# Kernel tuning notes

Measured on AMD Instinct MI355X. Metric: run time of the kernel, lower is better.

The kernel has to match this reference:

```python
import jax, jax.numpy as jnp
import numpy as np

B, S, Q, D = 8, 2048, 2048, 1024  # additive path requires S == Q


def setup_inputs() -> dict:
    key = jax.random.key(0)
    ks = jax.random.split(key, 5)
    def glorot(k, shape):
        fan_in, fan_out = shape[0], shape[1]
        limit = np.sqrt(6.0 / (fan_in + fan_out)).astype(np.float32)
        return jax.random.uniform(k, shape, jnp.float32, -limit, limit)
    return {
        "source": jax.random.normal(ks[0], (B, S, D), jnp.float32),
        "query": jax.random.normal(ks[1], (B, Q, D), jnp.float32),
        "kernel": glorot(ks[2], (S, Q)),
        "wk_kernel": glorot(ks[3], (D, Q)),
        "wq_kernel": glorot(ks[4], (S, D)),
    }


def reference(source, query, kernel, wk_kernel, wq_kernel):
    # query permuted to (B, D, Q) as in call()
    q_t = jnp.transpose(query, (0, 2, 1))
    # additive similarity: tanh(Wk . Source + Wq . Query) . kernel
    f_att = (jnp.einsum("bsd,dq->bsq", source, wk_kernel)
             + jnp.einsum("sd,bdq->bsq", wq_kernel, q_t))  # (B, S, Q)
    sim = jnp.einsum("bsq,qt->bst", jnp.tanh(f_att), kernel)  # (B, S, Q)
    sm = jax.nn.softmax(sim, axis=-1)  # softmax over last axis (Keras default)
    # sm_t = permute(sm, (0,2,1)); result = batch_dot(sm_t, Source)
    return jnp.einsum("bsq,bsd->bqd", sm, source)  # (B, Q, D)
```

## Files before the change

kernel.cpp:

```cpp
#include <hip/hip_runtime.h>
#include <hip/hip_bf16.h>
#include <stdint.h>

typedef unsigned short u16;

#define B_ 8
#define S_ 2048
#define Q_ 2048
#define D_ 1024
#define T_ 2048

typedef __attribute__((ext_vector_type(8))) short short8;
typedef __attribute__((ext_vector_type(16))) float f32x16;

__device__ __forceinline__ u16 f2b(float f) {
  union { float f; uint32_t u; } x; x.f = f;
  uint32_t r = x.u + 0x7fffu + ((x.u >> 16) & 1u);
  return (u16)(r >> 16);
}
__device__ __forceinline__ float b2f(u16 h) {
  union { uint32_t u; float f; } x; x.u = ((uint32_t)h) << 16;
  return x.f;
}
__device__ __forceinline__ float tanh_fast(float x) {
  return 1.0f - 2.0f / (__expf(2.0f * x) + 1.0f);
}
__device__ __forceinline__ void async16(const void* g, void* l) {
  __builtin_amdgcn_global_load_lds(
      (const __attribute__((address_space(1))) void*)g,
      (__attribute__((address_space(3))) void*)l, 16, 0, 0);
}

__global__ void cast_f32_bf16_k(const float* __restrict__ in, u16* __restrict__ out, int n4) {
  int i = blockIdx.x * 256 + threadIdx.x;
  if (i >= n4) return;
  float4 v = ((const float4*)in)[i];
  uint32_t lo = (uint32_t)f2b(v.x) | ((uint32_t)f2b(v.y) << 16);
  uint32_t hi = (uint32_t)f2b(v.z) | ((uint32_t)f2b(v.w) << 16);
  ((uint2*)out)[i] = make_uint2(lo, hi);
}

__global__ void transpose_f32_bf16_v(const float* __restrict__ in, u16* __restrict__ out,
                                     int R, int C) {
  __shared__ u16 t[64 * 72];
  int z = blockIdx.z;
  const float* pin = in + (size_t)z * R * C;
  u16* pout = out + (size_t)z * R * C;
  int c0 = blockIdx.x * 64, r0 = blockIdx.y * 64;
  int tid = threadIdx.x;
  int rr = tid >> 4, c4 = (tid & 15) * 4;
#pragma unroll
  for (int p = 0; p < 4; ++p) {
    int r = p * 16 + rr;
    float4 v = *(const float4*)&pin[(size_t)(r0 + r) * C + c0 + c4];
    t[(c4 + 0) * 72 + r] = f2b(v.x);
    t[(c4 + 1) * 72 + r] = f2b(v.y);
    t[(c4 + 2) * 72 + r] = f2b(v.z);
    t[(c4 + 3) * 72 + r] = f2b(v.w);
  }
  __syncthreads();
  int ct = tid >> 3, r8 = (tid & 7) * 8;
#pragma unroll
  for (int p = 0; p < 2; ++p) {
    int c = p * 32 + ct;
    uint2 lo = *(const uint2*)&t[c * 72 + r8];
    uint2 hi = *(const uint2*)&t[c * 72 + r8 + 4];
    *(uint4*)&pout[(size_t)(c0 + c) * R + r0 + r8] = make_uint4(lo.x, lo.y, hi.x, hi.y);
  }
}

__global__ void src_prep_v(const float* __restrict__ in, u16* __restrict__ outc,
                           u16* __restrict__ outT) {
  __shared__ u16 t[64 * 72];
  int z = blockIdx.z;
  const float* pin = in + (size_t)z * S_ * D_;
  u16* pc = outc + (size_t)z * S_ * D_;
  u16* pt = outT + (size_t)z * S_ * D_;
  int c0 = blockIdx.x * 64, r0 = blockIdx.y * 64;
  int tid = threadIdx.x;
  int rr = tid >> 4, c4 = (tid & 15) * 4;
#pragma unroll
  for (int p = 0; p < 4; ++p) {
    int r = p * 16 + rr;
    float4 v = *(const float4*)&pin[(size_t)(r0 + r) * D_ + c0 + c4];
    u16 b0 = f2b(v.x), b1 = f2b(v.y), b2 = f2b(v.z), b3 = f2b(v.w);
    uint2 pk;
    pk.x = (uint32_t)b0 | ((uint32_t)b1 << 16);
    pk.y = (uint32_t)b2 | ((uint32_t)b3 << 16);
    *(uint2*)&pc[(size_t)(r0 + r) * D_ + c0 + c4] = pk;
    t[(c4 + 0) * 72 + r] = b0;
    t[(c4 + 1) * 72 + r] = b1;
    t[(c4 + 2) * 72 + r] = b2;
    t[(c4 + 3) * 72 + r] = b3;
  }
  __syncthreads();
  int ct = tid >> 3, r8 = (tid & 7) * 8;
#pragma unroll
  for (int p = 0; p < 2; ++p) {
    int c = p * 32 + ct;
    uint2 lo = *(const uint2*)&t[c * 72 + r8];
    uint2 hi = *(const uint2*)&t[c * 72 + r8 + 4];
    *(uint4*)&pt[(size_t)(c0 + c) * S_ + r0 + r8] = make_uint4(lo.x, lo.y, hi.x, hi.y);
  }
}

__global__ void scale_srcT_k(u16* __restrict__ srcT, const float* __restrict__ l) {
  size_t i = (size_t)blockIdx.x * 256 + threadIdx.x;
  size_t e0 = i * 8;
  int s8 = (int)(e0 & (S_ - 1));
  int bb = (int)(e0 / ((size_t)D_ * S_));
  const float* lp = l + (size_t)bb * S_ + s8;
  float4 l0 = *(const float4*)lp;
  float4 l1 = *(const float4*)(lp + 4);
  uint4 raw = *(uint4*)&srcT[e0];
  uint32_t w[4] = {raw.x, raw.y, raw.z, raw.w};
  float li[8] = {l0.x, l0.y, l0.z, l0.w, l1.x, l1.y, l1.z, l1.w};
  uint32_t o[4];
#pragma unroll
  for (int k = 0; k < 4; ++k) {
    float a = b2f((u16)(w[k] & 0xffffu)) / li[2 * k];
    float b = b2f((u16)(w[k] >> 16)) / li[2 * k + 1];
    o[k] = (uint32_t)f2b(a) | ((uint32_t)f2b(b) << 16);
  }
  *(uint4*)&srcT[e0] = make_uint4(o[0], o[1], o[2], o[3]);
}

__global__ __launch_bounds__(512, 2) void gemm256_k(
    const u16* __restrict__ A1, long lda1, long bsA1,
    const u16* __restrict__ B1, long ldb1, long bsB1,
    const u16* __restrict__ A2, long lda2, long bsA2,
    const u16* __restrict__ B2, long ldb2, long bsB2,
    void* __restrict__ Cv, long ldc, long bsC,
    int K, int Srows, int nTerms, int mode, float* __restrict__ lsum) {
  __shared__ __align__(16) u16 lds[65536];

  const int tid = threadIdx.x;
  const int w = tid >> 6, lane = tid & 63;
  const int wr = w >> 2, wc = w & 3;
  const int l31 = lane & 31, hi = lane >> 5;

  const int gx = gridDim.x;
  const int nwg = gx * (int)gridDim.y;
  int lid = blockIdx.y * gx + blockIdx.x;
  if ((nwg & 7) == 0) lid = (lid & 7) * (nwg >> 3) + (lid >> 3);
  const int bn = lid % gx, bm = lid / gx;
  const int n0 = bn * 256, m0 = bm * 256;
  const int b = m0 / Srows;
  const int s0 = m0 - b * Srows;

  const int ktiles = K >> 6;
  const int ktlog = __ffs(ktiles) - 1;
  const int ktmask = ktiles - 1;
  const int NT = nTerms * ktiles;

  const u16* gA1 = A1 + (size_t)bsA1 * b + (size_t)s0 * lda1;
  const u16* gB1 = B1 + (size_t)bsB1 * b + (size_t)n0 * ldb1;
  const u16* gA2 = (nTerms > 1) ? (A2 + (size_t)bsA2 * b + (size_t)s0 * lda2) : gA1;
  const u16* gB2 = (nTerms > 1) ? (B2 + (size_t)bsB2 * b + (size_t)n0 * ldb2) : gB1;

  const int lrow = lane >> 3, lslot = lane & 7;
  const int gsl = (lslot ^ lrow) << 3;

  auto STG = [&](int tile, int isB, int half) {
    if (tile >= NT) return;
    const int term = tile >> ktlog;
    const int kt = (tile & ktmask) << 6;
    const u16* g = isB ? (term ? gB2 : gB1) : (term ? gA2 : gA1);
    const long ld = isB ? (term ? ldb2 : ldb1) : (term ? lda2 : lda1);
    u16* lb = lds + ((tile & 1) << 15) + (isB << 14);
#pragma unroll
    for (int is = 0; is < 2; ++is) {
      const int rh0 = is * 64 + w * 8;
      const int r0 = isB ? (half * 32 + (rh0 & 31) + ((rh0 >> 5) << 6))
                         : (half * 64 + (rh0 & 63) + ((rh0 >> 6) << 7));
      async16(g + (size_t)(r0 + lrow) * ld + kt + gsl, lb + r0 * 64);
    }
  };

  f32x16 acc[4][2];
#pragma unroll
  for (int x = 0; x < 4; ++x)
#pragma unroll
    for (int y = 0; y < 2; ++y)
#pragma unroll
      for (int r = 0; r < 16; ++r) acc[x][y][r] = 0.0f;

  u16* bufXA = lds;
  u16* bufXB = lds + 16384;
  u16* bufYA = lds + 32768;
  u16* bufYB = lds + 49152;

  const int aR = (wr * 128 + l31) * 64;
  const int bR = (wc * 64 + l31) * 64;
  int soff[4];
#pragma unroll
  for (int kk = 0; kk < 4; ++kk)
    soff[kk] = ((((kk << 1) | hi) ^ (l31 & 7)) << 3);

  short8 av[2][4], bv[4];

#define RD_A(bufA, mh)                                                        \
  _Pragma("unroll") for (int m = 0; m < 2; ++m)                               \
  _Pragma("unroll") for (int kk = 0; kk < 4; ++kk)                            \
      av[m][kk] = *(const short8*)&(bufA)[aR + ((mh)*2 + m) * 2048 + soff[kk]];
#define RD_B(bufB, nh)                                                        \
  _Pragma("unroll") for (int kk = 0; kk < 4; ++kk)                            \
      bv[kk] = *(const short8*)&(bufB)[bR + (nh)*2048 + soff[kk]];
#define BAR                              \
  __builtin_amdgcn_sched_barrier(0);     \
  __builtin_amdgcn_s_barrier();          \
  __builtin_amdgcn_sched_barrier(0)
#define MFMA8(mh, nh)                                                         \
  __builtin_amdgcn_s_setprio(1);                                              \
  _Pragma("unroll") for (int kk = 0; kk < 4; ++kk)                            \
  _Pragma("unroll") for (int m = 0; m < 2; ++m)                               \
      acc[(mh)*2 + m][nh] = __builtin_amdgcn_mfma_f32_32x32x16_bf16(          \
          av[m][kk], bv[kk], acc[(mh)*2 + m][nh], 0, 0, 0);                   \
  __builtin_amdgcn_s_setprio(0)
#define VMC4                                         \
  asm volatile("s_waitcnt vmcnt(4)" ::: "memory");   \
  __builtin_amdgcn_sched_barrier(0)

  STG(0, 0, 0); STG(0, 1, 1); STG(0, 0, 1); STG(0, 1, 0);
  STG(1, 0, 0); STG(1, 1, 1);
  VMC4;
  BAR;

  const int niter = NT >> 1;
  for (int i = 0; i < niter; ++i) {
    const int u = 2 * i;
    RD_A(bufXA, 0); RD_B(bufXB, 0);
    STG(u + 1, 0, 1);
    BAR; MFMA8(0, 0); BAR;

    RD_B(bufXB, 1);
    STG(u + 1, 1, 0);
    BAR; MFMA8(0, 1); BAR;

    RD_A(bufXA, 1);
    STG(u + 2, 0, 0);
    BAR; MFMA8(1, 1); BAR;

    RD_B(bufXB, 0);
    STG(u + 2, 1, 1);
    BAR; MFMA8(1, 0);
    VMC4;
    BAR;

    RD_A(bufYA, 0); RD_B(bufYB, 0);
    STG(u + 2, 0, 1);
    BAR; MFMA8(0, 0); BAR;

    RD_B(bufYB, 1);
    STG(u + 2, 1, 0);
    BAR; MFMA8(0, 1); BAR;

    RD_A(bufYA, 1);
    STG(u + 3, 0, 0);
    BAR; MFMA8(1, 1); BAR;

    RD_B(bufYB, 0);
    STG(u + 3, 1, 1);
    BAR; MFMA8(1, 0);
    VMC4;
    BAR;
  }

  if (mode == 3) {
#pragma unroll
    for (int mi = 0; mi < 4; ++mi)
#pragma unroll
      for (int ni = 0; ni < 2; ++ni)
#pragma unroll
        for (int r = 0; r < 16; ++r) acc[mi][ni][r] = __expf(acc[mi][ni][r]);
    float* lrowp = lsum + (size_t)b * Srows + s0;
#pragma unroll
    for (int mi = 0; mi < 4; ++mi)
#pragma unroll
      for (int r = 0; r < 16; ++r) {
        float pv = acc[mi][0][r] + acc[mi][1][r];
        pv += __shfl_xor(pv, 1);
        pv += __shfl_xor(pv, 2);
        pv += __shfl_xor(pv, 4);
        pv += __shfl_xor(pv, 8);
        pv += __shfl_xor(pv, 16);
        if (l31 == 0) {
          const int row = wr * 128 + mi * 32 + (r & 3) + 8 * (r >> 2) + 4 * hi;
          atomicAdd(&lrowp[row], pv);
        }
      }
    u16* gP = (u16*)Cv + (size_t)bsC * b + (size_t)n0 * ldc + s0;
    __syncthreads();
#pragma unroll
    for (int p = 0; p < 2; ++p) {
      if ((wc >> 1) == p) {
#pragma unroll
        for (int mi = 0; mi < 4; ++mi)
#pragma unroll
          for (int ni = 0; ni < 2; ++ni) {
            const int tc = (wc & 1) * 64 + ni * 32 + l31;
#pragma unroll
            for (int g2 = 0; g2 < 4; ++g2) {
              const int sr = wr * 128 + mi * 32 + g2 * 8 + hi * 4;
              u16 p0 = f2b(acc[mi][ni][g2 * 4 + 0]);
              u16 p1 = f2b(acc[mi][ni][g2 * 4 + 1]);
              u16 p2 = f2b(acc[mi][ni][g2 * 4 + 2]);
              u16 p3 = f2b(acc[mi][ni][g2 * 4 + 3]);
              uint2 pk;
              pk.x = (uint32_t)p0 | ((uint32_t)p1 << 16);
              pk.y = (uint32_t)p2 | ((uint32_t)p3 << 16);
              *(uint2*)&lds[tc * 268 + sr] = pk;
            }
          }
      }
      __syncthreads();
#pragma unroll
      for (int j = 0; j < 8; ++j) {
        const int idx = j * 512 + tid;
        const int tt = idx >> 5, s8 = (idx & 31) * 8;
        uint2 lo = *(const uint2*)&lds[tt * 268 + s8];
        uint2 h2 = *(const uint2*)&lds[tt * 268 + s8 + 4];
        *(uint4*)&gP[(size_t)(p * 128 + tt) * ldc + s8] =
            make_uint4(lo.x, lo.y, h2.x, h2.y);
      }
      __syncthreads();
    }
    return;
  }

  const size_t cb = (size_t)bsC * b + (size_t)s0 * ldc + n0;
  if (mode == 2) {
    float* C = (float*)Cv + cb;
#pragma unroll
    for (int mi = 0; mi < 4; ++mi)
#pragma unroll
      for (int ni = 0; ni < 2; ++ni) {
        const int col = wc * 64 + ni * 32 + l31;
#pragma unroll
        for (int r = 0; r < 16; ++r) {
          const int row = wr * 128 + mi * 32 + (r & 3) + 8 * (r >> 2) + 4 * hi;
          C[(size_t)row * ldc + col] = acc[mi][ni][r];
        }
      }
  } else {
    u16* C = (u16*)Cv + cb;
#pragma unroll
    for (int mi = 0; mi < 4; ++mi)
#pragma unroll
      for (int ni = 0; ni < 2; ++ni) {
        const int col = wc * 64 + ni * 32 + l31;
#pragma unroll
        for (int r = 0; r < 16; ++r) {
          const int row = wr * 128 + mi * 32 + (r & 3) + 8 * (r >> 2) + 4 * hi;
          float v = acc[mi][ni][r];
          if (mode == 0) v = tanh_fast(v);
          C[(size_t)row * ldc + col] = f2b(v);
        }
      }
  }
}

#undef RD_A
#undef RD_B
#undef BAR
#undef MFMA8
#undef VMC4

extern "C" void kernel_launch(void* const* d_in, const int* in_sizes, int n_in,
                              void* d_out, int out_size, void* d_ws, size_t ws_size,
                              hipStream_t stream) {
  const float* src = (const float*)d_in[0];
  const float* qry = (const float*)d_in[1];
  const float* ker = (const float*)d_in[2];
  const float* wk  = (const float*)d_in[3];
  const float* wq  = (const float*)d_in[4];
  float* out = (float*)d_out;
  u16* ws = (u16*)d_ws;

  u16* srcb  = ws;
  u16* qryb  = srcb  + (size_t)B_ * S_ * D_;
  u16* wqb   = qryb  + (size_t)B_ * Q_ * D_;
  u16* wkT   = wqb   + (size_t)S_ * D_;
  u16* kerT  = wkT   + (size_t)D_ * Q_;
  u16* srcT  = kerT  + (size_t)Q_ * T_;
  u16* tanhT = srcT  + (size_t)B_ * D_ * S_;
  u16* PT    = tanhT + (size_t)B_ * S_ * Q_;
  float* l   = (float*)(PT + (size_t)B_ * T_ * S_);

  dim3 tb(256);

  cast_f32_bf16_k<<<(B_ * Q_ * D_) / 1024, 256, 0, stream>>>(qry, qryb, (B_ * Q_ * D_) / 4);
  cast_f32_bf16_k<<<(S_ * D_) / 1024, 256, 0, stream>>>(wq, wqb, (S_ * D_) / 4);
  transpose_f32_bf16_v<<<dim3(Q_ / 64, D_ / 64, 1), tb, 0, stream>>>(wk, wkT, D_, Q_);
  transpose_f32_bf16_v<<<dim3(T_ / 64, Q_ / 64, 1), tb, 0, stream>>>(ker, kerT, Q_, T_);
  src_prep_v<<<dim3(D_ / 64, S_ / 64, B_), tb, 0, stream>>>(src, srcb, srcT);
  hipMemsetAsync(l, 0, (size_t)B_ * S_ * sizeof(float), stream);

  gemm256_k<<<dim3(Q_ / 256, (B_ * S_) / 256), 512, 0, stream>>>(
      srcb, D_, (long)S_ * D_,
      wkT, D_, 0,
      wqb, D_, 0,
      qryb, D_, (long)Q_ * D_,
      tanhT, Q_, (long)S_ * Q_,
      D_, S_, 2, 0, nullptr);

  gemm256_k<<<dim3(T_ / 256, (B_ * S_) / 256), 512, 0, stream>>>(
      tanhT, Q_, (long)S_ * Q_,
      kerT, Q_, 0,
      nullptr, 0, 0, nullptr, 0, 0,
      PT, S_, (long)T_ * S_,
      Q_, S_, 1, 3, l);

  scale_srcT_k<<<(B_ * D_ * S_) / (256 * 8), 256, 0, stream>>>(srcT, l);

  gemm256_k<<<dim3(D_ / 256, (B_ * T_) / 256), 512, 0, stream>>>(
      PT, S_, (long)T_ * S_,
      srcT, S_, (long)D_ * S_,
      nullptr, 0, 0, nullptr, 0, 0,
      out, D_, (long)T_ * D_,
      S_, T_, 1, 2, nullptr);
}
```

Before: 629.9 us.

## Pad LDS tile rows, peel the last K iteration, and tighten waitcnt scheduling

```diff
diff --git a/kernel.cpp b/kernel.cpp
--- a/kernel.cpp
+++ b/kernel.cpp
@@ -132,7 +132,7 @@
     const u16* __restrict__ B2, long ldb2, long bsB2,
     void* __restrict__ Cv, long ldc, long bsC,
     int K, int Srows, int nTerms, int mode, float* __restrict__ lsum) {
-  __shared__ __align__(16) u16 lds[65536];
+  __shared__ __align__(16) u16 lds[67584];
 
   const int tid = threadIdx.x;
   const int w = tid >> 6, lane = tid & 63;
@@ -167,13 +167,13 @@
     const int kt = (tile & ktmask) << 6;
     const u16* g = isB ? (term ? gB2 : gB1) : (term ? gA2 : gA1);
     const long ld = isB ? (term ? ldb2 : ldb1) : (term ? lda2 : lda1);
-    u16* lb = lds + ((tile & 1) << 15) + (isB << 14);
+    u16* lb = lds + (tile & 1) * 33792 + isB * 16896;
 #pragma unroll
     for (int is = 0; is < 2; ++is) {
       const int rh0 = is * 64 + w * 8;
       const int r0 = isB ? (half * 32 + (rh0 & 31) + ((rh0 >> 5) << 6))
                          : (half * 64 + (rh0 & 63) + ((rh0 >> 6) << 7));
-      async16(g + (size_t)(r0 + lrow) * ld + kt + gsl, lb + r0 * 64);
+      async16(g + (size_t)(r0 + lrow) * ld + kt + gsl, lb + (r0 >> 3) * 528);
     }
   };
 
@@ -186,12 +186,12 @@
       for (int r = 0; r < 16; ++r) acc[x][y][r] = 0.0f;
 
   u16* bufXA = lds;
-  u16* bufXB = lds + 16384;
-  u16* bufYA = lds + 32768;
-  u16* bufYB = lds + 49152;
-
-  const int aR = (wr * 128 + l31) * 64;
-  const int bR = (wc * 64 + l31) * 64;
+  u16* bufXB = lds + 16896;
+  u16* bufYA = lds + 33792;
+  u16* bufYB = lds + 50688;
+
+  const int aBase = (wr * 16 + (l31 >> 3)) * 528 + (l31 & 7) * 64;
+  const int bBase = (wc * 8 + (l31 >> 3)) * 528 + (l31 & 7) * 64;
   int soff[4];
 #pragma unroll
   for (int kk = 0; kk < 4; ++kk)
@@ -199,17 +199,25 @@
 
   short8 av[2][4], bv[4];
 
-#define RD_A(bufA, mh)                                                        \
-  _Pragma("unroll") for (int m = 0; m < 2; ++m)                               \
-  _Pragma("unroll") for (int kk = 0; kk < 4; ++kk)                            \
-      av[m][kk] = *(const short8*)&(bufA)[aR + ((mh)*2 + m) * 2048 + soff[kk]];
-#define RD_B(bufB, nh)                                                        \
-  _Pragma("unroll") for (int kk = 0; kk < 4; ++kk)                            \
-      bv[kk] = *(const short8*)&(bufB)[bR + (nh)*2048 + soff[kk]];
-#define BAR                              \
-  __builtin_amdgcn_sched_barrier(0);     \
-  __builtin_amdgcn_s_barrier();          \
-  __builtin_amdgcn_sched_barrier(0)
+#define RD_AB(bufA, bufB, mh, nh)                                               \
+  _Pragma("unroll") for (int kk = 0; kk < 4; ++kk) {                            \
+    av[0][kk] = *(const short8*)&(bufA)[aBase + ((mh)*2 + 0) * 2112 + soff[kk]];\
+    av[1][kk] = *(const short8*)&(bufA)[aBase + ((mh)*2 + 1) * 2112 + soff[kk]];\
+    bv[kk]    = *(const short8*)&(bufB)[bBase + (nh)*2112 + soff[kk]];          \
+  }
+#define RD_A(bufA, mh)                                                          \
+  _Pragma("unroll") for (int kk = 0; kk < 4; ++kk) {                            \
+    av[0][kk] = *(const short8*)&(bufA)[aBase + ((mh)*2 + 0) * 2112 + soff[kk]];\
+    av[1][kk] = *(const short8*)&(bufA)[aBase + ((mh)*2 + 1) * 2112 + soff[kk]];\
+  }
+#define RD_B(bufB, nh)                                                          \
+  _Pragma("unroll") for (int kk = 0; kk < 4; ++kk)                              \
+      bv[kk] = *(const short8*)&(bufB)[bBase + (nh)*2112 + soff[kk]];
+#define BAR __builtin_amdgcn_s_barrier()
+#define SB0 __builtin_amdgcn_sched_barrier(0)
+#define LGKM0 asm volatile("s_waitcnt lgkmcnt(0)")
+#define VMC4 asm volatile("s_waitcnt vmcnt(4)" ::: "memory")
+#define VMC0 asm volatile("s_waitcnt vmcnt(0)" ::: "memory")
 #define MFMA8(mh, nh)                                                         \
   __builtin_amdgcn_s_setprio(1);                                              \
   _Pragma("unroll") for (int kk = 0; kk < 4; ++kk)                            \
@@ -217,53 +225,109 @@
       acc[(mh)*2 + m][nh] = __builtin_amdgcn_mfma_f32_32x32x16_bf16(          \
           av[m][kk], bv[kk], acc[(mh)*2 + m][nh], 0, 0, 0);                   \
   __builtin_amdgcn_s_setprio(0)
-#define VMC4                                         \
-  asm volatile("s_waitcnt vmcnt(4)" ::: "memory");   \
-  __builtin_amdgcn_sched_barrier(0)
 
   STG(0, 0, 0); STG(0, 1, 1); STG(0, 0, 1); STG(0, 1, 0);
   STG(1, 0, 0); STG(1, 1, 1);
   VMC4;
-  BAR;
+  BAR; SB0;
 
   const int niter = NT >> 1;
-  for (int i = 0; i < niter; ++i) {
+  for (int i = 0; i + 1 < niter; ++i) {
     const int u = 2 * i;
-    RD_A(bufXA, 0); RD_B(bufXB, 0);
+    RD_AB(bufXA, bufXB, 0, 0);
     STG(u + 1, 0, 1);
-    BAR; MFMA8(0, 0); BAR;
+    BAR; LGKM0; SB0;
+    MFMA8(0, 0);
+    BAR;
 
     RD_B(bufXB, 1);
     STG(u + 1, 1, 0);
-    BAR; MFMA8(0, 1); BAR;
+    BAR; LGKM0; SB0;
+    MFMA8(0, 1);
+    BAR;
 
     RD_A(bufXA, 1);
     STG(u + 2, 0, 0);
-    BAR; MFMA8(1, 1); BAR;
+    BAR; LGKM0; SB0;
+    MFMA8(1, 1);
+    BAR;
 
     RD_B(bufXB, 0);
     STG(u + 2, 1, 1);
-    BAR; MFMA8(1, 0);
+    BAR; LGKM0; SB0;
+    MFMA8(1, 0);
     VMC4;
-    BAR;
-
-    RD_A(bufYA, 0); RD_B(bufYB, 0);
+    BAR; SB0;
+
+    RD_AB(bufYA, bufYB, 0, 0);
     STG(u + 2, 0, 1);
-    BAR; MFMA8(0, 0); BAR;
+    BAR; LGKM0; SB0;
+    MFMA8(0, 0);
+    BAR;
 
     RD_B(bufYB, 1);
     STG(u + 2, 1, 0);
-    BAR; MFMA8(0, 1); BAR;
+    BAR; LGKM0; SB0;
+    MFMA8(0, 1);
+    BAR;
 
     RD_A(bufYA, 1);
     STG(u + 3, 0, 0);
-    BAR; MFMA8(1, 1); BAR;
+    BAR; LGKM0; SB0;
+    MFMA8(1, 1);
+    BAR;
 
     RD_B(bufYB, 0);
     STG(u + 3, 1, 1);
-    BAR; MFMA8(1, 0);
+    BAR; LGKM0; SB0;
+    MFMA8(1, 0);
     VMC4;
-    BAR;
+    BAR; SB0;
+  }
+
+  {
+    const int u = NT - 2;
+    RD_AB(bufXA, bufXB, 0, 0);
+    STG(u + 1, 0, 1);
+    BAR; LGKM0; SB0;
+    MFMA8(0, 0);
+    BAR;
+
+    RD_B(bufXB, 1);
+    STG(u + 1, 1, 0);
+    BAR; LGKM0; SB0;
+    MFMA8(0, 1);
+    BAR;
+
+    RD_A(bufXA, 1);
+    BAR; LGKM0; SB0;
+    MFMA8(1, 1);
+    BAR;
+
+    RD_B(bufXB, 0);
+    BAR; LGKM0; SB0;
+    MFMA8(1, 0);
+    VMC0;
+    BAR; SB0;
+
+    RD_AB(bufYA, bufYB, 0, 0);
+    BAR; LGKM0; SB0;
+    MFMA8(0, 0);
+    BAR;
+
+    RD_B(bufYB, 1);
+    BAR; LGKM0; SB0;
+    MFMA8(0, 1);
+    BAR;
+
+    RD_A(bufYA, 1);
+    BAR; LGKM0; SB0;
+    MFMA8(1, 1);
+    BAR;
+
+    RD_B(bufYB, 0);
+    BAR; LGKM0; SB0;
+    MFMA8(1, 0);
   }
 
   if (mode == 3) {
@@ -360,11 +424,15 @@
   }
 }
 
+#undef RD_AB
 #undef RD_A
 #undef RD_B
 #undef BAR
+#undef SB0
+#undef LGKM0
+#undef VMC4
+#undef VMC0
 #undef MFMA8
-#undef VMC4
 
 extern "C" void kernel_launch(void* const* d_in, const int* in_sizes, int n_in,
                               void* d_out, int out_size, void* d_ws, size_t ws_size,
```

Result: slower. 654.7 us (+3.9%).

## Reorganize LDS layout to fragment order and software-pipeline LDS reads with MFMA

Applied to the files above, without the earlier changes.

```diff
diff --git a/kernel.cpp b/kernel.cpp
--- a/kernel.cpp
+++ b/kernel.cpp
@@ -158,22 +158,21 @@
   const u16* gA2 = (nTerms > 1) ? (A2 + (size_t)bsA2 * b + (size_t)s0 * lda2) : gA1;
   const u16* gB2 = (nTerms > 1) ? (B2 + (size_t)bsB2 * b + (size_t)n0 * ldb2) : gB1;
 
-  const int lrow = lane >> 3, lslot = lane & 7;
-  const int gsl = (lslot ^ lrow) << 3;
-
   auto STG = [&](int tile, int isB, int half) {
     if (tile >= NT) return;
     const int term = tile >> ktlog;
     const int kt = (tile & ktmask) << 6;
     const u16* g = isB ? (term ? gB2 : gB1) : (term ? gA2 : gA1);
     const long ld = isB ? (term ? ldb2 : ldb1) : (term ? lda2 : lda1);
-    u16* lb = lds + ((tile & 1) << 15) + (isB << 14);
+    u16* lb = lds + (tile & 1) * 32768 + isB * 16384;
 #pragma unroll
     for (int is = 0; is < 2; ++is) {
-      const int rh0 = is * 64 + w * 8;
-      const int r0 = isB ? (half * 32 + (rh0 & 31) + ((rh0 >> 5) << 6))
-                         : (half * 64 + (rh0 & 63) + ((rh0 >> 6) << 7));
-      async16(g + (size_t)(r0 + lrow) * ld + kt + gsl, lb + r0 * 64);
+      const int bi = is * 8 + w;
+      const int kk = (bi >> 1) & 3;
+      const int s = isB ? (half + ((bi & 1) << 1) + ((bi >> 3) << 2))
+                        : (half * 2 + (bi & 1) + ((bi >> 3) << 2));
+      async16(g + (size_t)(s * 32 + l31) * ld + kt + kk * 16 + hi * 8,
+              lb + s * 2048 + kk * 512);
     }
   };
 
@@ -190,80 +189,114 @@
   u16* bufYA = lds + 32768;
   u16* bufYB = lds + 49152;
 
-  const int aR = (wr * 128 + l31) * 64;
-  const int bR = (wc * 64 + l31) * 64;
-  int soff[4];
-#pragma unroll
-  for (int kk = 0; kk < 4; ++kk)
-    soff[kk] = ((((kk << 1) | hi) ^ (l31 & 7)) << 3);
-
-  short8 av[2][4], bv[4];
-
-#define RD_A(bufA, mh)                                                        \
-  _Pragma("unroll") for (int m = 0; m < 2; ++m)                               \
-  _Pragma("unroll") for (int kk = 0; kk < 4; ++kk)                            \
-      av[m][kk] = *(const short8*)&(bufA)[aR + ((mh)*2 + m) * 2048 + soff[kk]];
-#define RD_B(bufB, nh)                                                        \
-  _Pragma("unroll") for (int kk = 0; kk < 4; ++kk)                            \
-      bv[kk] = *(const short8*)&(bufB)[bR + (nh)*2048 + soff[kk]];
-#define BAR                              \
-  __builtin_amdgcn_sched_barrier(0);     \
-  __builtin_amdgcn_s_barrier();          \
-  __builtin_amdgcn_sched_barrier(0)
-#define MFMA8(mh, nh)                                                         \
-  __builtin_amdgcn_s_setprio(1);                                              \
-  _Pragma("unroll") for (int kk = 0; kk < 4; ++kk)                            \
-  _Pragma("unroll") for (int m = 0; m < 2; ++m)                               \
-      acc[(mh)*2 + m][nh] = __builtin_amdgcn_mfma_f32_32x32x16_bf16(          \
-          av[m][kk], bv[kk], acc[(mh)*2 + m][nh], 0, 0, 0);                   \
+  const int lof = lane * 8;
+
+  short8 av0[2][4], av1[2][4], bv0x[4], bv0y[4], bv1[4];
+
+#define RD_A0(buf)                                                             \
+  _Pragma("unroll") for (int m = 0; m < 2; ++m)                                \
+  _Pragma("unroll") for (int kk = 0; kk < 4; ++kk)                             \
+      av0[m][kk] = *(const short8*)&(buf)[(wr * 4 + m) * 2048 + kk * 512 + lof];
+#define RD_A1(buf)                                                             \
+  _Pragma("unroll") for (int m = 0; m < 2; ++m)                                \
+  _Pragma("unroll") for (int kk = 0; kk < 4; ++kk)                             \
+      av1[m][kk] = *(const short8*)&(buf)[(wr * 4 + 2 + m) * 2048 + kk * 512 + lof];
+#define RD_B0(buf, dst)                                                        \
+  _Pragma("unroll") for (int kk = 0; kk < 4; ++kk)                             \
+      dst[kk] = *(const short8*)&(buf)[(wc * 2) * 2048 + kk * 512 + lof];
+#define RD_B1(buf)                                                             \
+  _Pragma("unroll") for (int kk = 0; kk < 4; ++kk)                             \
+      bv1[kk] = *(const short8*)&(buf)[(wc * 2 + 1) * 2048 + kk * 512 + lof];
+#define BAR __builtin_amdgcn_s_barrier()
+#define SB0 __builtin_amdgcn_sched_barrier(0)
+#define LGKM0 asm volatile("s_waitcnt lgkmcnt(0)" ::: "memory")
+#define VMC4 asm volatile("s_waitcnt vmcnt(4)" ::: "memory")
+#define VMC2 asm volatile("s_waitcnt vmcnt(2)" ::: "memory")
+#define VMC0 asm volatile("s_waitcnt vmcnt(0)" ::: "memory")
+#define MFMA8(avs, bvs, mh, bp)                                                \
+  __builtin_amdgcn_s_setprio(1);                                               \
+  _Pragma("unroll") for (int kk = 0; kk < 4; ++kk)                             \
+  _Pragma("unroll") for (int m = 0; m < 2; ++m)                                \
+      acc[(mh)*2 + m][bp] = __builtin_amdgcn_mfma_f32_32x32x16_bf16(           \
+          avs[m][kk], bvs[kk], acc[(mh)*2 + m][bp], 0, 0, 0);                  \
   __builtin_amdgcn_s_setprio(0)
-#define VMC4                                         \
-  asm volatile("s_waitcnt vmcnt(4)" ::: "memory");   \
-  __builtin_amdgcn_sched_barrier(0)
-
-  STG(0, 0, 0); STG(0, 1, 1); STG(0, 0, 1); STG(0, 1, 0);
+
+  STG(0, 0, 0); STG(0, 1, 0); STG(0, 0, 1); STG(0, 1, 1);
   STG(1, 0, 0); STG(1, 1, 1);
   VMC4;
-  BAR;
+  BAR; SB0;
+  RD_A0(bufXA); RD_B0(bufXB, bv0x);
 
   const int niter = NT >> 1;
-  for (int i = 0; i < niter; ++i) {
+  for (int i = 0; i + 1 < niter; ++i) {
     const int u = 2 * i;
-    RD_A(bufXA, 0); RD_B(bufXB, 0);
+    LGKM0; SB0;
+    RD_B1(bufXB);
+    MFMA8(av0, bv0x, 0, 0);
     STG(u + 1, 0, 1);
-    BAR; MFMA8(0, 0); BAR;
-
-    RD_B(bufXB, 1);
+    BAR;
+    LGKM0; SB0;
+    RD_A1(bufXA);
+    MFMA8(av0, bv1, 0, 1);
     STG(u + 1, 1, 0);
-    BAR; MFMA8(0, 1); BAR;
-
-    RD_A(bufXA, 1);
+    BAR;
+    LGKM0; SB0;
+    MFMA8(av1, bv1, 1, 1);
     STG(u + 2, 0, 0);
-    BAR; MFMA8(1, 1); BAR;
-
-    RD_B(bufXB, 0);
+    VMC2; BAR; SB0;
+    RD_A0(bufYA); RD_B0(bufYB, bv0y);
+    MFMA8(av1, bv0x, 1, 0);
     STG(u + 2, 1, 1);
-    BAR; MFMA8(1, 0);
-    VMC4;
-    BAR;
-
-    RD_A(bufYA, 0); RD_B(bufYB, 0);
+    BAR;
+    LGKM0; SB0;
+    RD_B1(bufYB);
+    MFMA8(av0, bv0y, 0, 0);
     STG(u + 2, 0, 1);
-    BAR; MFMA8(0, 0); BAR;
-
-    RD_B(bufYB, 1);
+    BAR;
+    LGKM0; SB0;
+    RD_A1(bufYA);
+    MFMA8(av0, bv1, 0, 1);
     STG(u + 2, 1, 0);
-    BAR; MFMA8(0, 1); BAR;
-
-    RD_A(bufYA, 1);
+    BAR;
+    LGKM0; SB0;
+    MFMA8(av1, bv1, 1, 1);
     STG(u + 3, 0, 0);
-    BAR; MFMA8(1, 1); BAR;
-
-    RD_B(bufYB, 0);
+    VMC2; BAR; SB0;
+    RD_A0(bufXA); RD_B0(bufXB, bv0x);
+    MFMA8(av1, bv0y, 1, 0);
     STG(u + 3, 1, 1);
-    BAR; MFMA8(1, 0);
-    VMC4;
-    BAR;
+    BAR;
+  }
+
+  {
+    LGKM0; SB0;
+    RD_B1(bufXB);
+    MFMA8(av0, bv0x, 0, 0);
+    STG(NT - 1, 0, 1);
+    BAR;
+    LGKM0; SB0;
+    RD_A1(bufXA);
+    MFMA8(av0, bv1, 0, 1);
+    STG(NT - 1, 1, 0);
+    BAR;
+    LGKM0; SB0;
+    MFMA8(av1, bv1, 1, 1);
+    VMC0; BAR; SB0;
+    RD_A0(bufYA); RD_B0(bufYB, bv0y);
+    MFMA8(av1, bv0x, 1, 0);
+    BAR;
+    LGKM0; SB0;
+    RD_B1(bufYB);
+    MFMA8(av0, bv0y, 0, 0);
+    BAR;
+    LGKM0; SB0;
+    RD_A1(bufYA);
+    MFMA8(av0, bv1, 0, 1);
+    BAR;
+    LGKM0; SB0;
+    MFMA8(av1, bv1, 1, 1);
+    BAR;
+    MFMA8(av1, bv0y, 1, 0);
   }
 
   if (mode == 3) {
@@ -360,11 +393,17 @@
   }
 }
 
-#undef RD_A
-#undef RD_B
+#undef RD_A0
+#undef RD_A1
+#undef RD_B0
+#undef RD_B1
 #undef BAR
+#undef SB0
+#undef LGKM0
+#undef VMC4
+#undef VMC2
+#undef VMC0
 #undef MFMA8
-#undef VMC4
 
 extern "C" void kernel_launch(void* const* d_in, const int* in_sizes, int n_in,
                               void* d_out, int out_size, void* d_ws, size_t ws_size,
```

Result: slower. 815.2 us (+29.4%).
